# Kernel tuning notes

Measured on AMD Instinct MI355X. Metric: run time of the kernel, lower is better.

Reference implementation:

```python
import jax, jax.numpy as jnp
import numpy as np

QUERY_DIM = 1024
KEY_DIM = 768
NUM_HEADS = 16
HEAD_DIM = QUERY_DIM // NUM_HEADS
SCALE = HEAD_DIM ** -0.5


def setup_inputs() -> dict:
    key = jax.random.key(0)
    ks = jax.random.split(key, 11)
    B, Nq, Nk = 4, 4096, 1024
    s_q = QUERY_DIM ** -0.5
    s_k = KEY_DIM ** -0.5
    return {
        "query": jax.random.normal(ks[0], (B, Nq, QUERY_DIM), jnp.float32),
        "key": jax.random.normal(ks[1], (B, Nk, KEY_DIM), jnp.float32),
        "value": jax.random.normal(ks[2], (B, Nk, KEY_DIM), jnp.float32),
        "Wq": jax.random.normal(ks[3], (QUERY_DIM, QUERY_DIM), jnp.float32) * s_q,
        "bq": jnp.zeros((QUERY_DIM,), jnp.float32),
        "Wk": jax.random.normal(ks[4], (KEY_DIM, QUERY_DIM), jnp.float32) * s_k,
        "bk": jnp.zeros((QUERY_DIM,), jnp.float32),
        "Wv": jax.random.normal(ks[5], (KEY_DIM, QUERY_DIM), jnp.float32) * s_k,
        "bv": jnp.zeros((QUERY_DIM,), jnp.float32),
        "Wo": jax.random.normal(ks[6], (QUERY_DIM, QUERY_DIM), jnp.float32) * s_q,
        "bo": jnp.zeros((QUERY_DIM,), jnp.float32),
    }


def reference(query, key, value, Wq, bq, Wk, bk, Wv, bv, Wo, bo):
    B, Nq, _ = query.shape
    Nk = key.shape[1]
    # projections to (B, H, N, d)
    q = (query @ Wq + bq).reshape(B, Nq, NUM_HEADS, HEAD_DIM).transpose(0, 2, 1, 3)
    k = (key @ Wk + bk).reshape(B, Nk, NUM_HEADS, HEAD_DIM).transpose(0, 2, 1, 3)
    v = (value @ Wv + bv).reshape(B, Nk, NUM_HEADS, HEAD_DIM).transpose(0, 2, 1, 3)
    attn = jnp.einsum("bhqd,bhkd->bhqk", q, k) * SCALE
    attn = jax.nn.softmax(attn, axis=-1)
    out = jnp.einsum("bhqk,bhkd->bhqd", attn, v)
    out = out.transpose(0, 2, 1, 3).reshape(B, Nq, QUERY_DIM)
    return out @ Wo + bo
```

## Files before the change

### kernel.cpp

```cpp
#include <hip/hip_runtime.h>
#include <hip/hip_bf16.h>
#include <stdint.h>


typedef unsigned short u16;
typedef __attribute__((ext_vector_type(8))) short short8;
typedef __attribute__((ext_vector_type(4))) float f32x4;

#define B_SZ 4
#define NQ   4096
#define NK   1024
#define QDIM 1024
#define KDIM 768
#define NH   16
#define HD   64
#define QSCALE (0.125f * 1.44269504f)

__device__ __forceinline__ u16 f2bf(float f) {
  union { float f; uint32_t u; } v; v.f = f;
  uint32_t u = v.u;
  return (u16)((u + 0x7FFFu + ((u >> 16) & 1u)) >> 16);
}

__device__ __forceinline__ uint32_t pk2(float a, float b) {
  union { __hip_bfloat162 h; uint32_t u; } cv;
  cv.h = __float22bfloat162_rn(float2{a, b});
  return cv.u;
}

__device__ __forceinline__ float fexp2(float x) {
  return exp2f(x);
}

__device__ __forceinline__ void async16(u16* lds, const u16* g) {
  __builtin_amdgcn_global_load_lds(
      (__attribute__((address_space(1))) void*)(g),
      (__attribute__((address_space(3))) void*)(lds), 16, 0, 0);
}

__global__ __launch_bounds__(256) void f32_to_bf16_k(const float* __restrict__ in,
                                                     u16* __restrict__ out, int n4) {
  int i = blockIdx.x * 256 + threadIdx.x;
  if (i < n4) {
    f32x4 v = ((const f32x4*)in)[i];
    uint2 o = {pk2(v.x, v.y), pk2(v.z, v.w)};
    ((uint2*)out)[i] = o;
  }
}

__global__ __launch_bounds__(256) void f32_to_bf16_2k(const float* __restrict__ a,
                                                      const float* __restrict__ b,
                                                      u16* __restrict__ oa,
                                                      u16* __restrict__ ob, int n4) {
  int i = blockIdx.x * 256 + threadIdx.x;
  const float* in = blockIdx.y ? b : a;
  u16* out = blockIdx.y ? ob : oa;
  if (i < n4) {
    f32x4 v = ((const f32x4*)in)[i];
    uint2 o = {pk2(v.x, v.y), pk2(v.z, v.w)};
    ((uint2*)out)[i] = o;
  }
}

__global__ __launch_bounds__(256) void transpose_bf16_k(const float* __restrict__ W,
                                                        u16* __restrict__ Wt,
                                                        int K, int N) {
  __shared__ float t[32][33];
  int tx = threadIdx.x & 31, ty = threadIdx.x >> 5;
  int nb = blockIdx.x * 32, kb = blockIdx.y * 32;
#pragma unroll
  for (int i = 0; i < 4; ++i)
    t[ty + i * 8][tx] = W[(size_t)(kb + ty + i * 8) * N + nb + tx];
  __syncthreads();
#pragma unroll
  for (int i = 0; i < 4; ++i)
    Wt[(size_t)(nb + ty + i * 8) * K + kb + tx] = f2bf(t[tx][ty + i * 8]);
}

__global__ __launch_bounds__(256) void gemm_bt(const u16* __restrict__ A,
                                               const u16* __restrict__ Bt,
                                               const float* __restrict__ bias,
                                               float* __restrict__ Cf,
                                               u16* __restrict__ Cb,
                                               int M, int N, int K, int out_bf16,
                                               float scale) {
  __shared__ __align__(16) u16 Al[128 * 64];
  __shared__ __align__(16) u16 Bl[128 * 64];
  const int tid = threadIdx.x;
  const int w = tid >> 6, lane = tid & 63;
  const int g = lane >> 4, l15 = lane & 15;
  const int sw = l15 & 7;
  const int mbase = blockIdx.x * 128, nbase = blockIdx.y * 128;
  const int wm = (w & 1) * 64, wn = (w >> 1) * 64;

  f32x4 zero4 = {0.f, 0.f, 0.f, 0.f};
  f32x4 acc[4][4];
#pragma unroll
  for (int i = 0; i < 4; ++i)
#pragma unroll
    for (int j = 0; j < 4; ++j) acc[i][j] = zero4;

  for (int kb = 0; kb < K; kb += 64) {
#pragma unroll
    for (int i = 0; i < 4; ++i) {
      int cbase = w * 256 + i * 64;
      int c = cbase + lane;
      int row = c >> 3;
      int kc8 = ((c & 7) ^ (row & 7)) * 8;
      async16(&Al[cbase * 8], A + (size_t)(mbase + row) * K + kb + kc8);
      async16(&Bl[cbase * 8], Bt + (size_t)(nbase + row) * K + kb + kc8);
    }
    __syncthreads();
#pragma unroll
    for (int ks = 0; ks < 2; ++ks) {
      short8 af[4], bf[4];
#pragma unroll
      for (int mt = 0; mt < 4; ++mt)
        af[mt] = *(const short8*)&Al[(wm + mt * 16 + l15) * 64 + ((ks * 4 + g) ^ sw) * 8];
#pragma unroll
      for (int nt = 0; nt < 4; ++nt)
        bf[nt] = *(const short8*)&Bl[(wn + nt * 16 + l15) * 64 + ((ks * 4 + g) ^ sw) * 8];
#pragma unroll
      for (int mt = 0; mt < 4; ++mt)
#pragma unroll
        for (int nt = 0; nt < 4; ++nt)
          acc[mt][nt] = __builtin_amdgcn_mfma_f32_16x16x32_bf16(af[mt], bf[nt],
                                                                acc[mt][nt], 0, 0, 0);
    }
    __syncthreads();
  }

#pragma unroll
  for (int nt = 0; nt < 4; ++nt) {
    int col = nbase + wn + nt * 16 + l15;
    float bv = bias[col];
#pragma unroll
    for (int mt = 0; mt < 4; ++mt)
#pragma unroll
      for (int r = 0; r < 4; ++r) {
        int row = mbase + wm + mt * 16 + g * 4 + r;
        float v = (acc[mt][nt][r] + bv) * scale;
        if (out_bf16) Cb[(size_t)row * N + col] = f2bf(v);
        else          Cf[(size_t)row * N + col] = v;
      }
  }
}

__global__ __launch_bounds__(256) void gemm_kv(const u16* __restrict__ kA,
                                               const u16* __restrict__ vA,
                                               const u16* __restrict__ Wk,
                                               const u16* __restrict__ Wv,
                                               const float* __restrict__ bk,
                                               const float* __restrict__ bv,
                                               u16* __restrict__ Kp,
                                               u16* __restrict__ VT,
                                               int M, int N, int K) {
  __shared__ __align__(16) u16 Al[128 * 64];
  __shared__ __align__(16) u16 Bl[128 * 64];
  const int ct = blockIdx.z;
  const u16* A  = ct ? vA : kA;
  const u16* Bt = ct ? Wv : Wk;
  const float* bias = ct ? bv : bk;
  const int tid = threadIdx.x;
  const int w = tid >> 6, lane = tid & 63;
  const int g = lane >> 4, l15 = lane & 15;
  const int sw = l15 & 7;
  const int mbase = blockIdx.x * 128, nbase = blockIdx.y * 128;
  const int wm = (w & 1) * 64, wn = (w >> 1) * 64;

  f32x4 zero4 = {0.f, 0.f, 0.f, 0.f};
  f32x4 acc[4][4];
#pragma unroll
  for (int i = 0; i < 4; ++i)
#pragma unroll
    for (int j = 0; j < 4; ++j) acc[i][j] = zero4;

  for (int kb = 0; kb < K; kb += 64) {
#pragma unroll
    for (int i = 0; i < 4; ++i) {
      int cbase = w * 256 + i * 64;
      int c = cbase + lane;
      int row = c >> 3;
      int kc8 = ((c & 7) ^ (row & 7)) * 8;
      async16(&Al[cbase * 8], A + (size_t)(mbase + row) * K + kb + kc8);
      async16(&Bl[cbase * 8], Bt + (size_t)(nbase + row) * K + kb + kc8);
    }
    __syncthreads();
#pragma unroll
    for (int ks = 0; ks < 2; ++ks) {
      short8 af[4], bf[4];
#pragma unroll
      for (int mt = 0; mt < 4; ++mt)
        af[mt] = *(const short8*)&Al[(wm + mt * 16 + l15) * 64 + ((ks * 4 + g) ^ sw) * 8];
#pragma unroll
      for (int nt = 0; nt < 4; ++nt)
        bf[nt] = *(const short8*)&Bl[(wn + nt * 16 + l15) * 64 + ((ks * 4 + g) ^ sw) * 8];
      if (ct) {
#pragma unroll
        for (int nt = 0; nt < 4; ++nt)
#pragma unroll
          for (int mt = 0; mt < 4; ++mt)
            acc[nt][mt] = __builtin_amdgcn_mfma_f32_16x16x32_bf16(bf[nt], af[mt],
                                                                  acc[nt][mt], 0, 0, 0);
      } else {
#pragma unroll
        for (int mt = 0; mt < 4; ++mt)
#pragma unroll
          for (int nt = 0; nt < 4; ++nt)
            acc[mt][nt] = __builtin_amdgcn_mfma_f32_16x16x32_bf16(af[mt], bf[nt],
                                                                  acc[mt][nt], 0, 0, 0);
      }
    }
    __syncthreads();
  }

  if (ct) {
#pragma unroll
    for (int mt = 0; mt < 4; ++mt) {
      int m = mbase + wm + mt * 16 + l15;
#pragma unroll
      for (int nt = 0; nt < 4; ++nt)
#pragma unroll
        for (int r = 0; r < 4; ++r) {
          int n = nbase + wn + nt * 16 + g * 4 + r;
          VT[(size_t)n * M + m] = f2bf(acc[nt][mt][r] + bias[n]);
        }
    }
  } else {
#pragma unroll
    for (int nt = 0; nt < 4; ++nt) {
      int col = nbase + wn + nt * 16 + l15;
      float bvv = bias[col];
#pragma unroll
      for (int mt = 0; mt < 4; ++mt)
#pragma unroll
        for (int r = 0; r < 4; ++r) {
          int row = mbase + wm + mt * 16 + g * 4 + r;
          Kp[(size_t)row * N + col] = f2bf(acc[mt][nt][r] + bvv);
        }
    }
  }
}

__global__ __launch_bounds__(256) void attn_kernel(const u16* __restrict__ Qp,
                                                   const u16* __restrict__ Kp,
                                                   const u16* __restrict__ VT,
                                                   u16* __restrict__ AO) {
  __shared__ __align__(16) u16 K_lds[64 * 64];
  __shared__ __align__(16) u16 Vt_lds[64 * 64];
  __shared__ __align__(16) u16 P_lds[4][32 * 64];

  const int tid = threadIdx.x;
  const int w = tid >> 6, lane = tid & 63;
  const int g = lane >> 4, l15 = lane & 15;
  const int sw = l15 & 7;
  const int bh = blockIdx.y, b = bh >> 4, h = bh & 15;
  const int qrow0 = blockIdx.x * 128 + w * 32;
  const int MT = B_SZ * NK;

  short8 ones8;
#pragma unroll
  for (int j = 0; j < 8; ++j) ones8[j] = (short)0x3F80;

  short8 qf[2][2];
#pragma unroll
  for (int qt = 0; qt < 2; ++qt)
#pragma unroll
    for (int ks = 0; ks < 2; ++ks) {
      size_t row = (size_t)(b * NQ + qrow0 + qt * 16 + l15);
      qf[qt][ks] = *(const short8*)(Qp + row * QDIM + h * HD + ks * 32 + g * 8);
    }

  f32x4 zero4 = {0.f, 0.f, 0.f, 0.f};
  f32x4 o4[4][2];
  f32x4 lacc[2];
#pragma unroll
  for (int dt = 0; dt < 4; ++dt)
#pragma unroll
    for (int qt = 0; qt < 2; ++qt) o4[dt][qt] = zero4;
  lacc[0] = zero4; lacc[1] = zero4;

  for (int kc = 0; kc < NK / 64; ++kc) {
    const u16* Ksrc  = Kp + (size_t)(b * NK + kc * 64) * QDIM + h * HD;
    const u16* Vtsrc = VT + (size_t)(h * HD) * MT + b * NK + kc * 64;
#pragma unroll
    for (int i = 0; i < 2; ++i) {
      int cbase = (w * 2 + i) * 64;
      int c = cbase + lane;
      int row = c >> 3;
      int kc8 = ((c & 7) ^ (row & 7)) * 8;
      async16(&K_lds[cbase * 8],  Ksrc  + (size_t)row * QDIM + kc8);
      async16(&Vt_lds[cbase * 8], Vtsrc + (size_t)row * MT   + kc8);
    }
    __syncthreads();

    f32x4 sc[4][2];
#pragma unroll
    for (int mt = 0; mt < 4; ++mt)
#pragma unroll
      for (int qt = 0; qt < 2; ++qt) sc[mt][qt] = zero4;
#pragma unroll
    for (int ks = 0; ks < 2; ++ks) {
      short8 kf[4];
#pragma unroll
      for (int mt = 0; mt < 4; ++mt)
        kf[mt] = *(const short8*)&K_lds[(mt * 16 + l15) * 64 + ((ks * 4 + g) ^ sw) * 8];
#pragma unroll
      for (int mt = 0; mt < 4; ++mt)
#pragma unroll
        for (int qt = 0; qt < 2; ++qt)
          sc[mt][qt] = __builtin_amdgcn_mfma_f32_16x16x32_bf16(kf[mt], qf[qt][ks],
                                                               sc[mt][qt], 0, 0, 0);
    }

#pragma unroll
    for (int qt = 0; qt < 2; ++qt) {
#pragma unroll
      for (int mt = 0; mt < 4; ++mt) {
        float p0 = fexp2(sc[mt][qt][0]);
        float p1 = fexp2(sc[mt][qt][1]);
        float p2 = fexp2(sc[mt][qt][2]);
        float p3 = fexp2(sc[mt][qt][3]);
        uint2 pk = {pk2(p0, p1), pk2(p2, p3)};
        *(uint2*)&P_lds[w][(qt * 16 + l15) * 64 +
                           (((mt * 2) + (g >> 1)) ^ sw) * 8 + (g & 1) * 4] = pk;
      }
    }

#pragma unroll
    for (int ks = 0; ks < 2; ++ks) {
      short8 vf[4], pb[2];
#pragma unroll
      for (int dt = 0; dt < 4; ++dt)
        vf[dt] = *(const short8*)&Vt_lds[(dt * 16 + l15) * 64 + ((ks * 4 + g) ^ sw) * 8];
#pragma unroll
      for (int qt = 0; qt < 2; ++qt)
        pb[qt] = *(const short8*)&P_lds[w][(qt * 16 + l15) * 64 + ((ks * 4 + g) ^ sw) * 8];
#pragma unroll
      for (int qt = 0; qt < 2; ++qt)
        lacc[qt] = __builtin_amdgcn_mfma_f32_16x16x32_bf16(ones8, pb[qt],
                                                           lacc[qt], 0, 0, 0);
#pragma unroll
      for (int dt = 0; dt < 4; ++dt)
#pragma unroll
        for (int qt = 0; qt < 2; ++qt)
          o4[dt][qt] = __builtin_amdgcn_mfma_f32_16x16x32_bf16(vf[dt], pb[qt],
                                                               o4[dt][qt], 0, 0, 0);
    }
    __syncthreads();
  }

#pragma unroll
  for (int qt = 0; qt < 2; ++qt) {
    float inv = 1.0f / lacc[qt][0];
    size_t row = (size_t)(b * NQ + qrow0 + qt * 16 + l15);
#pragma unroll
    for (int dt = 0; dt < 4; ++dt) {
      uint2 pk = {pk2(o4[dt][qt][0] * inv, o4[dt][qt][1] * inv),
                  pk2(o4[dt][qt][2] * inv, o4[dt][qt][3] * inv)};
      *(uint2*)(AO + row * QDIM + h * HD + dt * 16 + g * 4) = pk;
    }
  }
}

extern "C" void kernel_launch(void* const* d_in, const int* in_sizes, int n_in,
                              void* d_out, int out_size, void* d_ws, size_t ws_size,
                              hipStream_t stream) {
  const float* query = (const float*)d_in[0];
  const float* key   = (const float*)d_in[1];
  const float* value = (const float*)d_in[2];
  const float* Wq = (const float*)d_in[3];
  const float* bq = (const float*)d_in[4];
  const float* Wk = (const float*)d_in[5];
  const float* bk = (const float*)d_in[6];
  const float* Wv = (const float*)d_in[7];
  const float* bv = (const float*)d_in[8];
  const float* Wo = (const float*)d_in[9];
  const float* bo = (const float*)d_in[10];

  char* ws = (char*)d_ws;
  size_t off = 0;
  auto alloc = [&](size_t bytes) -> void* {
    void* p = ws + off;
    off += (bytes + 255) & ~(size_t)255;
    return p;
  };
  const size_t NQTOT = (size_t)B_SZ * NQ;
  const size_t NKTOT = (size_t)B_SZ * NK;
  u16* qbf = (u16*)alloc(NQTOT * QDIM * 2);
  u16* kbf = (u16*)alloc(NKTOT * KDIM * 2);
  u16* vbf = (u16*)alloc(NKTOT * KDIM * 2);
  u16* wqt = (u16*)alloc((size_t)QDIM * QDIM * 2);
  u16* wkt = (u16*)alloc((size_t)KDIM * QDIM * 2);
  u16* wvt = (u16*)alloc((size_t)KDIM * QDIM * 2);
  u16* wot = (u16*)alloc((size_t)QDIM * QDIM * 2);
  u16* Qp  = (u16*)alloc(NQTOT * QDIM * 2);
  u16* Kp  = (u16*)alloc(NKTOT * QDIM * 2);
  u16* VT  = (u16*)alloc((size_t)QDIM * NKTOT * 2);
  u16* AO  = qbf;

  {
    int n4 = (int)(NQTOT * QDIM / 4);
    f32_to_bf16_k<<<(n4 + 255) / 256, 256, 0, stream>>>(query, qbf, n4);
  }
  {
    int n4 = (int)(NKTOT * KDIM / 4);
    f32_to_bf16_2k<<<dim3((n4 + 255) / 256, 2), 256, 0, stream>>>(key, value, kbf,
                                                                  vbf, n4);
  }
  transpose_bf16_k<<<dim3(QDIM / 32, QDIM / 32), 256, 0, stream>>>(Wq, wqt, QDIM, QDIM);
  transpose_bf16_k<<<dim3(QDIM / 32, KDIM / 32), 256, 0, stream>>>(Wk, wkt, KDIM, QDIM);
  transpose_bf16_k<<<dim3(QDIM / 32, KDIM / 32), 256, 0, stream>>>(Wv, wvt, KDIM, QDIM);
  transpose_bf16_k<<<dim3(QDIM / 32, QDIM / 32), 256, 0, stream>>>(Wo, wot, QDIM, QDIM);

  gemm_bt<<<dim3(NQTOT / 128, QDIM / 128), 256, 0, stream>>>(
      qbf, wqt, bq, nullptr, Qp, (int)NQTOT, QDIM, QDIM, 1, QSCALE);
  gemm_kv<<<dim3(NKTOT / 128, QDIM / 128, 2), 256, 0, stream>>>(
      kbf, vbf, wkt, wvt, bk, bv, Kp, VT, (int)NKTOT, QDIM, KDIM);

  attn_kernel<<<dim3(NQ / 128, B_SZ * NH), 256, 0, stream>>>(Qp, Kp, VT, AO);

  gemm_bt<<<dim3(NQTOT / 128, QDIM / 128), 256, 0, stream>>>(
      AO, wot, bo, (float*)d_out, nullptr, (int)NQTOT, QDIM, QDIM, 0, 1.0f);

  (void)in_sizes; (void)n_in; (void)out_size; (void)ws_size;
}
```

Baseline: 430.8 us.

## Double-buffer K/V tiles in attention, add MFMA priority hints and fast exp/rcp

The attention kernel now keeps two LDS buffers for the K and V^T tiles. The next chunk's async global-to-LDS loads are issued before the current chunk is computed, and one barrier per iteration is dropped. Address arithmetic is hoisted out of the loop, s_setprio is raised around the MFMA groups, exp2f becomes the hardware exp2 builtin, and the final divide becomes a hardware reciprocal. The goal is to hide global load latency behind compute. The cost is twice the K/V LDS footprint, which may lower occupancy, and the builtins give up some accuracy on edge cases.

```diff
diff --git a/kernel.cpp b/kernel.cpp
--- a/kernel.cpp
+++ b/kernel.cpp
@@ -29,7 +29,7 @@
 }
 
 __device__ __forceinline__ float fexp2(float x) {
-  return exp2f(x);
+  return __builtin_amdgcn_exp2f(x);
 }
 
 __device__ __forceinline__ void async16(u16* lds, const u16* g) {
@@ -246,8 +246,8 @@
                                                    const u16* __restrict__ Kp,
                                                    const u16* __restrict__ VT,
                                                    u16* __restrict__ AO) {
-  __shared__ __align__(16) u16 K_lds[64 * 64];
-  __shared__ __align__(16) u16 Vt_lds[64 * 64];
+  __shared__ __align__(16) u16 K_lds[2][64 * 64];
+  __shared__ __align__(16) u16 Vt_lds[2][64 * 64];
   __shared__ __align__(16) u16 P_lds[4][32 * 64];
 
   const int tid = threadIdx.x;
@@ -258,6 +258,23 @@
   const int qrow0 = blockIdx.x * 128 + w * 32;
   const int MT = B_SZ * NK;
 
+  const int cbase0 = (w * 2 + 0) * 64;
+  const int cbase1 = (w * 2 + 1) * 64;
+  const int c0 = cbase0 + lane, c1 = cbase1 + lane;
+  const int row0 = c0 >> 3, kc80 = ((c0 & 7) ^ (row0 & 7)) * 8;
+  const int row1 = c1 >> 3, kc81 = ((c1 & 7) ^ (row1 & 7)) * 8;
+
+  const u16* kp0 = Kp + (size_t)(b * NK + row0) * QDIM + h * HD + kc80;
+  const u16* kp1 = Kp + (size_t)(b * NK + row1) * QDIM + h * HD + kc81;
+  const u16* vp0 = VT + (size_t)(h * HD + row0) * MT + b * NK + kc80;
+  const u16* vp1 = VT + (size_t)(h * HD + row1) * MT + b * NK + kc81;
+
+  const int rb = l15 * 64;
+  const int cs0 = (g ^ sw) * 8;
+  const int cs1 = ((4 + g) ^ sw) * 8;
+  const int pwb = rb + (((g >> 1) ^ (sw & 1)) * 8) + (g & 1) * 4;
+  const int pms = sw & 6;
+
   short8 ones8;
 #pragma unroll
   for (int j = 0; j < 8; ++j) ones8[j] = (short)0x3F80;
@@ -280,37 +297,52 @@
     for (int qt = 0; qt < 2; ++qt) o4[dt][qt] = zero4;
   lacc[0] = zero4; lacc[1] = zero4;
 
+  async16(&K_lds[0][cbase0 * 8], kp0);
+  async16(&K_lds[0][cbase1 * 8], kp1);
+  async16(&Vt_lds[0][cbase0 * 8], vp0);
+  async16(&Vt_lds[0][cbase1 * 8], vp1);
+  kp0 += 64 * QDIM; kp1 += 64 * QDIM; vp0 += 64; vp1 += 64;
+  __syncthreads();
+
+  int cur = 0;
   for (int kc = 0; kc < NK / 64; ++kc) {
-    const u16* Ksrc  = Kp + (size_t)(b * NK + kc * 64) * QDIM + h * HD;
-    const u16* Vtsrc = VT + (size_t)(h * HD) * MT + b * NK + kc * 64;
-#pragma unroll
-    for (int i = 0; i < 2; ++i) {
-      int cbase = (w * 2 + i) * 64;
-      int c = cbase + lane;
-      int row = c >> 3;
-      int kc8 = ((c & 7) ^ (row & 7)) * 8;
-      async16(&K_lds[cbase * 8],  Ksrc  + (size_t)row * QDIM + kc8);
-      async16(&Vt_lds[cbase * 8], Vtsrc + (size_t)row * MT   + kc8);
-    }
-    __syncthreads();
+    if (kc + 1 < NK / 64) {
+      int nb = cur ^ 1;
+      async16(&K_lds[nb][cbase0 * 8], kp0);
+      async16(&K_lds[nb][cbase1 * 8], kp1);
+      async16(&Vt_lds[nb][cbase0 * 8], vp0);
+      async16(&Vt_lds[nb][cbase1 * 8], vp1);
+      kp0 += 64 * QDIM; kp1 += 64 * QDIM; vp0 += 64; vp1 += 64;
+    }
+    const u16* Kl = &K_lds[cur][0];
+    const u16* Vl = &Vt_lds[cur][0];
+    u16* Pl = &P_lds[w][0];
 
     f32x4 sc[4][2];
-#pragma unroll
-    for (int mt = 0; mt < 4; ++mt)
-#pragma unroll
-      for (int qt = 0; qt < 2; ++qt) sc[mt][qt] = zero4;
-#pragma unroll
-    for (int ks = 0; ks < 2; ++ks) {
+    {
       short8 kf[4];
 #pragma unroll
       for (int mt = 0; mt < 4; ++mt)
-        kf[mt] = *(const short8*)&K_lds[(mt * 16 + l15) * 64 + ((ks * 4 + g) ^ sw) * 8];
+        kf[mt] = *(const short8*)&Kl[mt * 1024 + rb + cs0];
+      __builtin_amdgcn_s_setprio(1);
 #pragma unroll
       for (int mt = 0; mt < 4; ++mt)
 #pragma unroll
         for (int qt = 0; qt < 2; ++qt)
-          sc[mt][qt] = __builtin_amdgcn_mfma_f32_16x16x32_bf16(kf[mt], qf[qt][ks],
+          sc[mt][qt] = __builtin_amdgcn_mfma_f32_16x16x32_bf16(kf[mt], qf[qt][0],
+                                                               zero4, 0, 0, 0);
+      __builtin_amdgcn_s_setprio(0);
+#pragma unroll
+      for (int mt = 0; mt < 4; ++mt)
+        kf[mt] = *(const short8*)&Kl[mt * 1024 + rb + cs1];
+      __builtin_amdgcn_s_setprio(1);
+#pragma unroll
+      for (int mt = 0; mt < 4; ++mt)
+#pragma unroll
+        for (int qt = 0; qt < 2; ++qt)
+          sc[mt][qt] = __builtin_amdgcn_mfma_f32_16x16x32_bf16(kf[mt], qf[qt][1],
                                                                sc[mt][qt], 0, 0, 0);
+      __builtin_amdgcn_s_setprio(0);
     }
 
 #pragma unroll
@@ -322,20 +354,21 @@
         float p2 = fexp2(sc[mt][qt][2]);
         float p3 = fexp2(sc[mt][qt][3]);
         uint2 pk = {pk2(p0, p1), pk2(p2, p3)};
-        *(uint2*)&P_lds[w][(qt * 16 + l15) * 64 +
-                           (((mt * 2) + (g >> 1)) ^ sw) * 8 + (g & 1) * 4] = pk;
+        *(uint2*)&Pl[qt * 1024 + pwb + ((mt * 2) ^ pms) * 8] = pk;
       }
     }
 
 #pragma unroll
     for (int ks = 0; ks < 2; ++ks) {
+      const int cs = ks ? cs1 : cs0;
       short8 vf[4], pb[2];
 #pragma unroll
       for (int dt = 0; dt < 4; ++dt)
-        vf[dt] = *(const short8*)&Vt_lds[(dt * 16 + l15) * 64 + ((ks * 4 + g) ^ sw) * 8];
+        vf[dt] = *(const short8*)&Vl[dt * 1024 + rb + cs];
 #pragma unroll
       for (int qt = 0; qt < 2; ++qt)
-        pb[qt] = *(const short8*)&P_lds[w][(qt * 16 + l15) * 64 + ((ks * 4 + g) ^ sw) * 8];
+        pb[qt] = *(const short8*)&Pl[qt * 1024 + rb + cs];
+      __builtin_amdgcn_s_setprio(1);
 #pragma unroll
       for (int qt = 0; qt < 2; ++qt)
         lacc[qt] = __builtin_amdgcn_mfma_f32_16x16x32_bf16(ones8, pb[qt],
@@ -346,13 +379,15 @@
         for (int qt = 0; qt < 2; ++qt)
           o4[dt][qt] = __builtin_amdgcn_mfma_f32_16x16x32_bf16(vf[dt], pb[qt],
                                                                o4[dt][qt], 0, 0, 0);
-    }
-    __syncthreads();
+      __builtin_amdgcn_s_setprio(0);
+    }
+    if (kc + 1 < NK / 64) __syncthreads();
+    cur ^= 1;
   }
 
 #pragma unroll
   for (int qt = 0; qt < 2; ++qt) {
-    float inv = 1.0f / lacc[qt][0];
+    float inv = __builtin_amdgcn_rcpf(lacc[qt][0]);
     size_t row = (size_t)(b * NQ + qrow0 + qt * 16 + l15);
 #pragma unroll
     for (int dt = 0; dt < 4; ++dt) {
```

Result: no change. 428.1 us (-0.6%).
